# Kernel tuning notes

Hardware: AMD Instinct MI355X
Metric: run time of the kernel (lower is better)

## Reference

```python
import jax, jax.numpy as jnp
import numpy as np
from jax import lax

B, T, U, V = 4, 256, 64, 1024   # batch, enc frames, max target len, vocab (blank=0)
F, H, HD, J = 80, 512, 512, 512  # feat dim, enc dim, dec dim, joint dim
NEG = -1e30


def setup_inputs() -> dict:
    key = jax.random.key(0)
    ks = jax.random.split(key, 10)
    inputs = jax.random.normal(ks[0], (B, T, F), dtype=jnp.float32)
    targets = jax.random.randint(ks[1], (B, U), 1, V, dtype=jnp.int32)  # labels exclude blank=0
    input_lengths = jax.random.randint(ks[2], (B,), T // 2, T + 1, dtype=jnp.int32)
    target_lengths = jax.random.randint(ks[3], (B,), U // 2, U + 1, dtype=jnp.int32)
    s = 0.02
    W_enc = jax.random.normal(ks[4], (F, H), dtype=jnp.float32) * s
    emb = jax.random.normal(ks[5], (V, HD), dtype=jnp.float32) * s
    W_jenc = jax.random.normal(ks[6], (H, J), dtype=jnp.float32) * s
    W_jdec = jax.random.normal(ks[7], (HD, J), dtype=jnp.float32) * s
    b_j = jnp.zeros((J,), dtype=jnp.float32)
    W_out = jax.random.normal(ks[8], (J, V), dtype=jnp.float32) * s
    b_out = jnp.zeros((V,), dtype=jnp.float32)
    return {"inputs": inputs, "W_enc": W_enc, "emb": emb, "W_jenc": W_jenc,
            "W_jdec": W_jdec, "b_j": b_j, "W_out": W_out, "b_out": b_out,
            "targets": targets, "input_lengths": input_lengths,
            "target_lengths": target_lengths}


def rnnt_loss(log_probs, targets, in_lens, tgt_lens):
    """RNN-T loss (blank=0, 'gather' variant: gather blank/label lps, then DP).
    log_probs: (B,T,U+1,V) log-softmaxed joint. Returns mean loss over batch."""
    Bq, Tq, U1, _ = log_probs.shape
    Uq = U1 - 1
    blank_lp = log_probs[..., 0]                                    # (B,T,U+1)
    lbl_lp = jnp.take_along_axis(
        log_probs[:, :, :Uq, :],
        jnp.broadcast_to(targets[:, None, :, None], (Bq, Tq, Uq, 1)),
        axis=3)[..., 0]                                             # (B,T,U)
    u_idx = jnp.arange(Uq)
    lbl_lp = jnp.where(u_idx[None, None, :] < tgt_lens[:, None, None], lbl_lp, NEG)

    def row(a, py):
        # a: (B,U+1) = alpha_prev + blank emission; py: (B,U) label lps this frame
        def step(c, x):
            a_u, py_prev = x
            c = jnp.logaddexp(a_u, c + py_prev)
            return c, c
        c0 = a[:, 0]
        _, rest = lax.scan(step, c0, (a[:, 1:].T, py.T))            # (U,B)
        return jnp.concatenate([c0[:, None], rest.T], axis=1)      # (B,U+1)

    # t=0 row: alpha[0,u] = cumsum of label lps at frame 0
    alpha0 = jnp.concatenate(
        [jnp.zeros((Bq, 1), log_probs.dtype),
         jnp.cumsum(lbl_lp[:, 0, :], axis=1)], axis=1)              # (B,U+1)

    def tstep(alpha_prev, x):
        blank_prev, py_t = x
        alpha = row(alpha_prev + blank_prev, py_t)
        return alpha, alpha

    xs = (jnp.swapaxes(blank_lp[:, :-1, :], 0, 1),                  # (T-1,B,U+1)
          jnp.swapaxes(lbl_lp[:, 1:, :], 0, 1))                    # (T-1,B,U)
    _, rest = lax.scan(tstep, alpha0, xs)
    alphas = jnp.concatenate([alpha0[None], rest], axis=0)          # (T,B,U+1)

    b = jnp.arange(Bq)
    t_last = in_lens - 1
    a_fin = alphas[t_last, b, tgt_lens] + blank_lp[b, t_last, tgt_lens]
    return -jnp.mean(a_fin)


def reference(inputs, W_enc, emb, W_jenc, W_jdec, b_j, W_out, b_out,
              targets, input_lengths, target_lengths):
    enc = inputs @ W_enc                                            # (B,T,H) encoder
    padded = jnp.concatenate(
        [jnp.zeros((targets.shape[0], 1), targets.dtype), targets], axis=1)
    dec = emb[padded]                                               # (B,U+1,HD) decoder
    e = enc @ W_jenc                                                # (B,T,J)
    d = dec @ W_jdec                                                # (B,U+1,J)
    h = jnp.tanh(e[:, :, None, :] + d[:, None, :, :] + b_j)        # (B,T,U+1,J)
    logits = h @ W_out + b_out                                      # (B,T,U+1,V)
    log_probs = jax.nn.log_softmax(logits, axis=-1)
    return rnnt_loss(log_probs, targets, input_lengths, target_lengths)
```

## Files before the change

### kernel.cpp

```cpp
#include <hip/hip_runtime.h>
#include <stdint.h>

#define NEGF (-1e30f)

typedef unsigned short ushort_t;
typedef unsigned char uchar_t;
typedef __attribute__((ext_vector_type(2))) long v2i64;
typedef __attribute__((ext_vector_type(4))) float f32x4;

constexpr int cB = 4, cT = 256, cU = 64, cU1 = 65, cV = 1024, cF = 80, cH = 512, cJ = 512;
constexpr int cM = cB * cT * cU1;
constexpr int cTU = cT * cU1;
constexpr float LOG2E = 1.4426950408889634f;

__device__ __forceinline__ float tanh_fast(float x){
  float t = x * x;
  float num = x * (27.f + t);
  float den = fmaf(9.f, t, 27.f);
  float r = num * __builtin_amdgcn_rcpf(den);
  return fminf(1.f, fmaxf(-1.f, r));
}

__device__ __forceinline__ float logadd2(float x, float y){
  float m = fmaxf(x, y);
  return m + __builtin_amdgcn_logf(1.f + __builtin_amdgcn_exp2f(-fabsf(x - y)));
}

__device__ __forceinline__ float wshr1(float x){
  return __int_as_float(__builtin_amdgcn_mov_dpp(__float_as_int(x),
                                                 0x138, 0xF, 0xF, true));
}

__device__ __forceinline__ int pk8(float a, float b, float c, float d){
  int v = __builtin_amdgcn_cvt_pk_fp8_f32(a, b, 0, false);
  v = __builtin_amdgcn_cvt_pk_fp8_f32(c, d, v, true);
  return v;
}

__global__ __launch_bounds__(256) void k_pre(
    const float* __restrict__ inputs,
    const float* __restrict__ W_enc, const float* __restrict__ W_jenc,
    const float* __restrict__ emb, const int* __restrict__ targets,
    const float* __restrict__ W_jdec, const float* __restrict__ b_j,
    float* __restrict__ dmatb, float* __restrict__ e,
    const float* __restrict__ W_out, uchar_t* __restrict__ WTf8,
    float* __restrict__ S, float* __restrict__ out_loss)
{
  __shared__ float sA[4][512];
  __shared__ float sIn[4][80];
  int bid = blockIdx.x;
  int tid = threadIdx.x;

  if (bid < 256){
    int m0 = bid * 4;
    for (int i = tid; i < 320; i += 256)
      sIn[i / 80][i % 80] = inputs[m0 * 80 + i];
    __syncthreads();
    int c0 = tid, c1 = tid + 256;
    float a00 = 0.f, a01 = 0.f, a10 = 0.f, a11 = 0.f;
    float a20 = 0.f, a21 = 0.f, a30 = 0.f, a31 = 0.f;
#pragma unroll 8
    for (int k = 0; k < 80; k++){
      float w0 = W_enc[(size_t)k * 512 + c0];
      float w1 = W_enc[(size_t)k * 512 + c1];
      a00 = fmaf(sIn[0][k], w0, a00); a01 = fmaf(sIn[0][k], w1, a01);
      a10 = fmaf(sIn[1][k], w0, a10); a11 = fmaf(sIn[1][k], w1, a11);
      a20 = fmaf(sIn[2][k], w0, a20); a21 = fmaf(sIn[2][k], w1, a21);
      a30 = fmaf(sIn[3][k], w0, a30); a31 = fmaf(sIn[3][k], w1, a31);
    }
    sA[0][c0] = a00; sA[0][c1] = a01;
    sA[1][c0] = a10; sA[1][c1] = a11;
    sA[2][c0] = a20; sA[2][c1] = a21;
    sA[3][c0] = a30; sA[3][c1] = a31;
    __syncthreads();
    float b00 = 0.f, b01 = 0.f, b10 = 0.f, b11 = 0.f;
    float b20 = 0.f, b21 = 0.f, b30 = 0.f, b31 = 0.f;
#pragma unroll 8
    for (int k = 0; k < 512; k++){
      float w0 = W_jenc[(size_t)k * 512 + c0];
      float w1 = W_jenc[(size_t)k * 512 + c1];
      b00 = fmaf(sA[0][k], w0, b00); b01 = fmaf(sA[0][k], w1, b01);
      b10 = fmaf(sA[1][k], w0, b10); b11 = fmaf(sA[1][k], w1, b11);
      b20 = fmaf(sA[2][k], w0, b20); b21 = fmaf(sA[2][k], w1, b21);
      b30 = fmaf(sA[3][k], w0, b30); b31 = fmaf(sA[3][k], w1, b31);
    }
    e[(size_t)(m0 + 0) * 512 + c0] = b00; e[(size_t)(m0 + 0) * 512 + c1] = b01;
    e[(size_t)(m0 + 1) * 512 + c0] = b10; e[(size_t)(m0 + 1) * 512 + c1] = b11;
    e[(size_t)(m0 + 2) * 512 + c0] = b20; e[(size_t)(m0 + 2) * 512 + c1] = b21;
    e[(size_t)(m0 + 3) * 512 + c0] = b30; e[(size_t)(m0 + 3) * 512 + c1] = b31;
  } else if (bid < 386){
    int id = bid - 256;
    int bx = id & 1, by = id >> 1;
    int m0 = by * 4;
    int col = bx * 256 + tid;
    for (int i = tid; i < 4 * 512; i += 256){
      int r = i >> 9, c = i & 511;
      int row = m0 + r;
      int b = row / cU1, u = row % cU1;
      int src = (u == 0) ? 0 : targets[b * cU + (u - 1)];
      sA[r][c] = emb[(size_t)src * cH + c];
    }
    __syncthreads();
    float a0 = 0.f, a1 = 0.f, a2 = 0.f, a3 = 0.f;
#pragma unroll 8
    for (int k = 0; k < 512; k++){
      float bv = W_jdec[(size_t)k * cJ + col];
      a0 = fmaf(sA[0][k], bv, a0);
      a1 = fmaf(sA[1][k], bv, a1);
      a2 = fmaf(sA[2][k], bv, a2);
      a3 = fmaf(sA[3][k], bv, a3);
    }
    float bb = b_j[col];
    dmatb[(size_t)(m0 + 0) * cJ + col] = a0 + bb;
    dmatb[(size_t)(m0 + 1) * cJ + col] = a1 + bb;
    dmatb[(size_t)(m0 + 2) * cJ + col] = a2 + bb;
    dmatb[(size_t)(m0 + 3) * cJ + col] = a3 + bb;
  } else if (bid < 418){
    int id = bid - 386;
    int bn = id & 3, ksp = id >> 2;
    int lane = tid & 63, nth = tid >> 6;
    int c16 = lane & 15, quad = lane >> 4;
    int jA = ksp * 64 + quad * 8;
#pragma unroll
    for (int i = 0; i < 4; i++){
      int nt16 = nth * 4 + i;
      int n = bn * 256 + nt16 * 16 + c16;
      unsigned int p[4];
#pragma unroll
      for (int h = 0; h < 4; h++){
        int j0 = jA + (h >> 1) * 32 + (h & 1) * 4;
        float w0 = W_out[(size_t)(j0 + 0) * cV + n] * 32.f;
        float w1 = W_out[(size_t)(j0 + 1) * cV + n] * 32.f;
        float w2 = W_out[(size_t)(j0 + 2) * cV + n] * 32.f;
        float w3 = W_out[(size_t)(j0 + 3) * cV + n] * 32.f;
        p[h] = (unsigned)pk8(w0, w1, w2, w3);
      }
      uint4 pack; pack.x = p[0]; pack.y = p[1]; pack.z = p[2]; pack.w = p[3];
      *(uint4*)(WTf8 + (((size_t)(bn * 8 + ksp) * 16 + nt16) * 64 + lane) * 16) = pack;
    }
  } else {
    int i = (bid - 418) * 1024 + tid * 4;
    float4 z; z.x = 0.f; z.y = 0.f; z.z = 0.f; z.w = 0.f;
    *(float4*)(S + i) = z;
    if (bid == 418 && tid == 0) out_loss[0] = 0.f;
  }
}

__global__ __launch_bounds__(256) void k_hf(const float* __restrict__ e,
                                            const float* __restrict__ dmatb,
                                            uchar_t* __restrict__ Hbf8){
  __shared__ uchar_t sH[16 * 520];
  int tid = threadIdx.x;
  int wid = tid >> 6, lane = tid & 63;
  int c16 = lane & 15, quad = lane >> 4;
  int bm = blockIdx.x;
  int bu = bm >> 1, thalf = bm & 1;
  int b = bu / cU1;
  int t0 = thalf * 128;

  float dj[8];
  const float4* dp = (const float4*)(dmatb + (size_t)bu * cJ + lane * 8);
  float4 dA = dp[0], dB = dp[1];
  dj[0] = dA.x; dj[1] = dA.y; dj[2] = dA.z; dj[3] = dA.w;
  dj[4] = dB.x; dj[5] = dB.y; dj[6] = dB.z; dj[7] = dB.w;

  const float* erow0 = e + ((size_t)(b * cT + t0)) * cJ + lane * 8;
  uchar_t* outb = Hbf8 + (size_t)bm * 65536 + lane * 16;

  for (int mg = 0; mg < 8; mg++){
#pragma unroll
    for (int rr = 0; rr < 4; rr++){
      int rloc = wid * 4 + rr;
      const float* ep = erow0 + ((size_t)(mg * 16 + rloc)) * cJ;
      float4 e0 = *(const float4*)ep;
      float4 e1 = *(const float4*)(ep + 4);
      int v0 = pk8(tanh_fast(e0.x + dj[0]), tanh_fast(e0.y + dj[1]),
                   tanh_fast(e0.z + dj[2]), tanh_fast(e0.w + dj[3]));
      int v1 = pk8(tanh_fast(e1.x + dj[4]), tanh_fast(e1.y + dj[5]),
                   tanh_fast(e1.z + dj[6]), tanh_fast(e1.w + dj[7]));
      uint2 pk; pk.x = (unsigned)v0; pk.y = (unsigned)v1;
      *(uint2*)(sH + rloc * 520 + lane * 8) = pk;
    }
    __syncthreads();
#pragma unroll
    for (int q = 0; q < 2; q++){
      int ksp = wid * 2 + q;
      uint2 lo = *(const uint2*)(sH + c16 * 520 + ksp * 64 + quad * 8);
      uint2 hi = *(const uint2*)(sH + c16 * 520 + ksp * 64 + 32 + quad * 8);
      uint4 pack; pack.x = lo.x; pack.y = lo.y; pack.z = hi.x; pack.w = hi.y;
      *(uint4*)(outb + ((size_t)ksp * 8 + mg) * 1024) = pack;
    }
    __syncthreads();
  }
}

__global__ __launch_bounds__(256, 3) void k_joint(
    const uchar_t* __restrict__ Hbf8, const uchar_t* __restrict__ WTf8,
    const float* __restrict__ b_out, const int* __restrict__ targets,
    float* __restrict__ S,
    float* __restrict__ blank_g, float* __restrict__ lbl_g)
{
  __shared__ float redS[2][128];

  int tid = threadIdx.x;
  int wid = tid >> 6, lane = tid & 63;
  int quad = lane >> 4, c16 = lane & 15;
  int wm = wid & 1, wn = wid >> 1;
  int bid = blockIdx.x;
  int bm = ((bid >> 6) << 3) + (bid & 7);
  int bn = (bid >> 3) & 7;
  int bu = bm >> 1, thalf = bm & 1;
  int b = bu / cU1, u = bu - b * cU1;
  int tg = (u < cU) ? targets[b * cU + u] : -1;
  int lin0 = bu * cT + thalf * 128;

  f32x4 acc[4][4];
#pragma unroll
  for (int i = 0; i < 4; i++)
#pragma unroll
    for (int j = 0; j < 4; j++)
      acc[i][j] = (f32x4){0.f, 0.f, 0.f, 0.f};

  const uchar_t* aP = Hbf8 + (size_t)bm * 65536 + (wm * 4) * 1024 + lane * 16;
  const uchar_t* bP = WTf8 + (size_t)(bn >> 1) * 131072 + ((bn & 1) * 8 + wn * 4) * 1024 + lane * 16;

  v2i64 afX[4], bfX[4], afY[4], bfY[4];
#pragma unroll
  for (int mt = 0; mt < 4; mt++) afX[mt] = *(const v2i64*)(aP + mt * 1024);
#pragma unroll
  for (int nt = 0; nt < 4; nt++) bfX[nt] = *(const v2i64*)(bP + nt * 1024);

#pragma unroll
  for (int k2 = 0; k2 < 4; k2++){
    {
      size_t kY = (size_t)(2 * k2 + 1);
#pragma unroll
      for (int mt = 0; mt < 4; mt++) afY[mt] = *(const v2i64*)(aP + kY * 8192 + mt * 1024);
#pragma unroll
      for (int nt = 0; nt < 4; nt++) bfY[nt] = *(const v2i64*)(bP + kY * 16384 + nt * 1024);
    }
#pragma unroll
    for (int h = 0; h < 2; h++)
#pragma unroll
      for (int mt = 0; mt < 4; mt++)
#pragma unroll
        for (int nt = 0; nt < 4; nt++)
          acc[mt][nt] = __builtin_amdgcn_mfma_f32_16x16x32_fp8_fp8(afX[mt][h], bfX[nt][h], acc[mt][nt], 0, 0, 0);
    if (k2 < 3){
      size_t kX = (size_t)(2 * k2 + 2);
#pragma unroll
      for (int mt = 0; mt < 4; mt++) afX[mt] = *(const v2i64*)(aP + kX * 8192 + mt * 1024);
#pragma unroll
      for (int nt = 0; nt < 4; nt++) bfX[nt] = *(const v2i64*)(bP + kX * 16384 + nt * 1024);
    }
#pragma unroll
    for (int h = 0; h < 2; h++)
#pragma unroll
      for (int mt = 0; mt < 4; mt++)
#pragma unroll
        for (int nt = 0; nt < 4; nt++)
          acc[mt][nt] = __builtin_amdgcn_mfma_f32_16x16x32_fp8_fp8(afY[mt][h], bfY[nt][h], acc[mt][nt], 0, 0, 0);
  }

  float bv[4];
#pragma unroll
  for (int nt = 0; nt < 4; nt++) bv[nt] = b_out[bn * 128 + (wn * 4 + nt) * 16 + c16] * LOG2E;

  bool ownL = (tg >= 0) && ((tg >> 7) == bn) && (((tg >> 6) & 1) == wn);
  int ntO = (tg >> 4) & 3;
  int tgc = tg & 15;
  const float descale2 = LOG2E / 32.f;

#pragma unroll
  for (int mt = 0; mt < 4; mt++){
#pragma unroll
    for (int r = 0; r < 4; r++){
      int rl = wm * 64 + mt * 16 + quad * 4 + r;
      float l[4];
#pragma unroll
      for (int nt = 0; nt < 4; nt++) l[nt] = fmaf(acc[mt][nt][r], descale2, bv[nt]);
      if (bn == 0 && wn == 0 && c16 == 0) blank_g[lin0 + rl] = l[0];
      if (ownL && c16 == tgc){
        float v = l[0];
#pragma unroll
        for (int k = 1; k < 4; k++) v = (ntO == k) ? l[k] : v;
        lbl_g[lin0 + rl] = v;
      }
      float s = __builtin_amdgcn_exp2f(l[0]) + __builtin_amdgcn_exp2f(l[1])
              + __builtin_amdgcn_exp2f(l[2]) + __builtin_amdgcn_exp2f(l[3]);
      s += __shfl_xor(s, 1, 64);
      s += __shfl_xor(s, 2, 64);
      s += __shfl_xor(s, 4, 64);
      s += __shfl_xor(s, 8, 64);
      if (c16 == 0) redS[wn][rl] = s;
    }
  }
  __syncthreads();
  if (tid < 128)
    atomicAdd(&S[lin0 + tid], redS[0][tid] + redS[1][tid]);
}

__global__ __launch_bounds__(256) void k_dp(
    const float* __restrict__ S, const float* __restrict__ blank_g,
    const float* __restrict__ lbl_g,
    const int* __restrict__ in_len, const int* __restrict__ tgt_len,
    float* __restrict__ out)
{
  __shared__ float sbb[cTU];
  __shared__ float slb[cTU];
  __shared__ float sS[256];
  int b = blockIdx.x;
  int tl  = tgt_len[b];
  size_t base = (size_t)b * cTU;
  for (int i = threadIdx.x; i < cTU / 4; i += 256){
    int row = i >> 6;
    if (row > tl) continue;
    float4 sv = ((const float4*)(S + base))[i];
    float4 bvv = ((const float4*)(blank_g + base))[i];
    float4 ls;
    ls.x = __builtin_amdgcn_logf(sv.x); ls.y = __builtin_amdgcn_logf(sv.y);
    ls.z = __builtin_amdgcn_logf(sv.z); ls.w = __builtin_amdgcn_logf(sv.w);
    float4 bo;
    bo.x = bvv.x - ls.x; bo.y = bvv.y - ls.y;
    bo.z = bvv.z - ls.z; bo.w = bvv.w - ls.w;
    ((float4*)sbb)[i] = bo;
    float4 lo;
    if (row < tl){
      float4 lv = ((const float4*)(lbl_g + base))[i];
      lo.x = lv.x - ls.x; lo.y = lv.y - ls.y;
      lo.z = lv.z - ls.z; lo.w = lv.w - ls.w;
    } else {
      lo.x = NEGF; lo.y = NEGF; lo.z = NEGF; lo.w = NEGF;
    }
    ((float4*)slb)[i] = lo;
  }
  __syncthreads();
  if (threadIdx.x >= 64) return;

  int u = threadIdx.x;
  int til = in_len[b] - 1;
  bool cap64 = (tl == 64);
  bool isTL = (u == tl);
  const float* pbu  = sbb + (u << 8);
  const float* pbu1 = sbb + (((u >= 1) ? u - 1 : 0) << 8);
  const float* plu1 = slb + (((u >= 1) ? u - 1 : 0) << 8);
  const float* plu2 = slb + (((u >= 2) ? u - 2 : 0) << 8);
  bool u1 = (u >= 1), u2 = (u >= 2);
  float fb = pbu[til];

  float A = (u == 0) ? 0.f : NEGF;
  float res = 0.f;

  auto ld = [&](const float* p, int i, bool ok) -> float {
    float x = p[i & 255];
    return (ok & ((unsigned)i < 256u)) ? x : NEGF;
  };

  int i0 = -u;
  float o0 = ld(pbu,  i0,     true);
  float o1 = ld(pbu,  i0 + 1, true);
  float o2 = ld(plu1, i0 + 1, u1);
  float o3 = ld(pbu1, i0 + 1, u1);
  float o4 = ld(plu1, i0 + 2, u1);
  float o5 = ld(plu2, i0 + 2, u2);

#pragma unroll 3
  for (int g = 0; g < 159; g++){
    float up1 = wshr1(A);
    float up2 = wshr1(up1);

    int i0n = i0 + 2;
    float n0 = ld(pbu,  i0n,     true);
    float n1 = ld(pbu,  i0n + 1, true);
    float n2 = ld(plu1, i0n + 1, u1);
    float n3 = ld(pbu1, i0n + 1, u1);
    float n4 = ld(plu1, i0n + 2, u1);
    float n5 = ld(plu2, i0n + 2, u2);

    float C0 = o0 + o1;
    float C1 = logadd2(o2 + o1, o3 + o4);
    float C2 = o5 + o4;

    float am0 = A + o0, am1 = up1 + o2;
    float Amid = logadd2(am0, am1);
    bool tv1 = ((unsigned)(i0 + 1) < 256u);
    Amid = tv1 ? Amid : NEGF;

    float a0 = A + C0, a1 = up1 + C1, a2 = up2 + C2;
    float m3 = fmaxf(fmaxf(a0, a1), a2);
    float s3 = __builtin_amdgcn_exp2f(a0 - m3) + __builtin_amdgcn_exp2f(a1 - m3)
             + __builtin_amdgcn_exp2f(a2 - m3);
    float Anew = m3 + __builtin_amdgcn_logf(s3);
    bool tv2 = ((unsigned)(i0 + 2) < 256u);
    Anew = tv2 ? Anew : NEGF;

    if (isTL && (i0 + 1) == til) res = Amid + fb;
    if (isTL && (i0 + 2) == til) res = Anew + fb;
    if (u == 63){
      if (tv1) sS[i0 + 1] = Amid;
      if (tv2) sS[i0 + 2] = Anew;
    }
    A = Anew;
    i0 = i0n;
    o0 = n0; o1 = n1; o2 = n2; o3 = n3; o4 = n4; o5 = n5;
  }

  if (cap64){
    const float* pb64 = sbb + (64 << 8);
    const float* pl63 = slb + (63 << 8);
    float A64 = sS[0] + pl63[0];
    for (int t = 1; t <= til; t++)
      A64 = logadd2(A64 + pb64[t - 1], sS[t] + pl63[t]);
    if (u == 0) res = A64 + pb64[til];
  }

  res += __shfl_xor(res, 1, 64);
  res += __shfl_xor(res, 2, 64);
  res += __shfl_xor(res, 4, 64);
  res += __shfl_xor(res, 8, 64);
  res += __shfl_xor(res, 16, 64);
  res += __shfl_xor(res, 32, 64);
  if (u == 0) atomicAdd(out, -0.17328679513998632f * res);
}

extern "C" void kernel_launch(void* const* d_in, const int* in_sizes, int n_in,
                              void* d_out, int out_size, void* d_ws, size_t ws_size,
                              hipStream_t stream)
{
  (void)in_sizes; (void)n_in; (void)out_size; (void)ws_size;
  const float* inputs = (const float*)d_in[0];
  const float* W_enc  = (const float*)d_in[1];
  const float* emb    = (const float*)d_in[2];
  const float* W_jenc = (const float*)d_in[3];
  const float* W_jdec = (const float*)d_in[4];
  const float* b_j    = (const float*)d_in[5];
  const float* W_out  = (const float*)d_in[6];
  const float* b_out  = (const float*)d_in[7];
  const int* targets  = (const int*)d_in[8];
  const int* in_len   = (const int*)d_in[9];
  const int* tgt_len  = (const int*)d_in[10];

  char* w = (char*)d_ws;
  auto alloc = [&](size_t bytes){ char* p = w; w += (bytes + 255) & ~(size_t)255; return p; };
  float* e       = (float*)alloc((size_t)1024 * 512 * 4);
  float* dmatb   = (float*)alloc((size_t)260 * 512 * 4);
  float* blank_g = (float*)alloc((size_t)cM * 4);
  float* lbl_g   = (float*)alloc((size_t)cM * 4);
  float* S       = (float*)alloc((size_t)cM * 4);
  uchar_t* Hbf8  = (uchar_t*)alloc((size_t)520 * 65536);
  uchar_t* WTf8  = (uchar_t*)alloc((size_t)4 * 131072);

  k_pre<<<483, 256, 0, stream>>>(inputs, W_enc, W_jenc, emb, targets, W_jdec, b_j,
                                 dmatb, e, W_out, WTf8, S, (float*)d_out);
  k_hf<<<520, 256, 0, stream>>>(e, dmatb, Hbf8);
  k_joint<<<4160, 256, 0, stream>>>(Hbf8, WTf8, b_out, targets, S, blank_g, lbl_g);
  k_dp<<<4, 256, 0, stream>>>(S, blank_g, lbl_g, in_len, tgt_len, (float*)d_out);
}
```

Measured before the change: 223.2 us.

## Precompute DP emission combinations cooperatively across block in phases

The anti-diagonal RNN-T alpha recurrence previously had one wavefront compute all emission sums (C0, C1, C2 and the logadd) inline on its serial chain. Now all 256 threads precompute these terms for 16 diagonal steps at a time into shared memory, and the single wavefront then runs only the recurrence on the precomputed values. The aim is to take the loads and the logadd off the serial critical path. In exchange it adds 10 phases of block-wide __syncthreads and extra shared-memory traffic.

```diff
diff --git a/kernel.cpp b/kernel.cpp
--- a/kernel.cpp
+++ b/kernel.cpp
@@ -306,13 +306,18 @@
     const int* __restrict__ in_len, const int* __restrict__ tgt_len,
     float* __restrict__ out)
 {
+  constexpr int G = 16;
+  constexpr int NPH = 10;
   __shared__ float sbb[cTU];
   __shared__ float slb[cTU];
   __shared__ float sS[256];
+  __shared__ float cC0[G * 64], cC1[G * 64], cC2[G * 64];
+  __shared__ float cOA[G * 64], cOB[G * 64];
+  int tid = threadIdx.x;
   int b = blockIdx.x;
   int tl  = tgt_len[b];
   size_t base = (size_t)b * cTU;
-  for (int i = threadIdx.x; i < cTU / 4; i += 256){
+  for (int i = tid; i < cTU / 4; i += 256){
     int row = i >> 6;
     if (row > tl) continue;
     float4 sv = ((const float4*)(S + base))[i];
@@ -335,18 +340,12 @@
     ((float4*)slb)[i] = lo;
   }
   __syncthreads();
-  if (threadIdx.x >= 64) return;
-
-  int u = threadIdx.x;
+
   int til = in_len[b] - 1;
   bool cap64 = (tl == 64);
+  int u = tid;
   bool isTL = (u == tl);
-  const float* pbu  = sbb + (u << 8);
-  const float* pbu1 = sbb + (((u >= 1) ? u - 1 : 0) << 8);
-  const float* plu1 = slb + (((u >= 1) ? u - 1 : 0) << 8);
-  const float* plu2 = slb + (((u >= 2) ? u - 2 : 0) << 8);
-  bool u1 = (u >= 1), u2 = (u >= 2);
-  float fb = pbu[til];
+  float fb = (tid < 64) ? sbb[(u << 8) + til] : 0.f;
 
   float A = (u == 0) ? 0.f : NEGF;
   float res = 0.f;
@@ -356,54 +355,67 @@
     return (ok & ((unsigned)i < 256u)) ? x : NEGF;
   };
 
-  int i0 = -u;
-  float o0 = ld(pbu,  i0,     true);
-  float o1 = ld(pbu,  i0 + 1, true);
-  float o2 = ld(plu1, i0 + 1, u1);
-  float o3 = ld(pbu1, i0 + 1, u1);
-  float o4 = ld(plu1, i0 + 2, u1);
-  float o5 = ld(plu2, i0 + 2, u2);
-
-#pragma unroll 3
-  for (int g = 0; g < 159; g++){
-    float up1 = wshr1(A);
-    float up2 = wshr1(up1);
-
-    int i0n = i0 + 2;
-    float n0 = ld(pbu,  i0n,     true);
-    float n1 = ld(pbu,  i0n + 1, true);
-    float n2 = ld(plu1, i0n + 1, u1);
-    float n3 = ld(pbu1, i0n + 1, u1);
-    float n4 = ld(plu1, i0n + 2, u1);
-    float n5 = ld(plu2, i0n + 2, u2);
-
-    float C0 = o0 + o1;
-    float C1 = logadd2(o2 + o1, o3 + o4);
-    float C2 = o5 + o4;
-
-    float am0 = A + o0, am1 = up1 + o2;
-    float Amid = logadd2(am0, am1);
-    bool tv1 = ((unsigned)(i0 + 1) < 256u);
-    Amid = tv1 ? Amid : NEGF;
-
-    float a0 = A + C0, a1 = up1 + C1, a2 = up2 + C2;
-    float m3 = fmaxf(fmaxf(a0, a1), a2);
-    float s3 = __builtin_amdgcn_exp2f(a0 - m3) + __builtin_amdgcn_exp2f(a1 - m3)
-             + __builtin_amdgcn_exp2f(a2 - m3);
-    float Anew = m3 + __builtin_amdgcn_logf(s3);
-    bool tv2 = ((unsigned)(i0 + 2) < 256u);
-    Anew = tv2 ? Anew : NEGF;
-
-    if (isTL && (i0 + 1) == til) res = Amid + fb;
-    if (isTL && (i0 + 2) == til) res = Anew + fb;
-    if (u == 63){
-      if (tv1) sS[i0 + 1] = Amid;
-      if (tv2) sS[i0 + 2] = Anew;
-    }
-    A = Anew;
-    i0 = i0n;
-    o0 = n0; o1 = n1; o2 = n2; o3 = n3; o4 = n4; o5 = n5;
-  }
+  for (int p = 0; p < NPH; p++){
+    for (int w = tid; w < G * 64; w += 256){
+      int gg = w >> 6, uu = w & 63;
+      int g = p * G + gg;
+      int i0 = 2 * g - uu;
+      bool v1 = (uu >= 1), v2 = (uu >= 2);
+      const float* pbu  = sbb + (uu << 8);
+      const float* pbu1 = sbb + ((v1 ? uu - 1 : 0) << 8);
+      const float* plu1 = slb + ((v1 ? uu - 1 : 0) << 8);
+      const float* plu2 = slb + ((v2 ? uu - 2 : 0) << 8);
+      float o0 = ld(pbu,  i0,     true);
+      float o1 = ld(pbu,  i0 + 1, true);
+      float o2 = ld(plu1, i0 + 1, v1);
+      float o3 = ld(pbu1, i0 + 1, v1);
+      float o4 = ld(plu1, i0 + 2, v1);
+      float o5 = ld(plu2, i0 + 2, v2);
+      cC0[w] = o0 + o1;
+      cC1[w] = logadd2(o2 + o1, o3 + o4);
+      cC2[w] = o5 + o4;
+      cOA[w] = o0;
+      cOB[w] = o2;
+    }
+    __syncthreads();
+    if (tid < 64){
+      float c0v = cC0[u], c1v = cC1[u], c2v = cC2[u];
+      float oAv = cOA[u], oBv = cOB[u];
+#pragma unroll
+      for (int gg = 0; gg < G; gg++){
+        int g = p * G + gg;
+        int nx = (gg + 1 < G) ? ((gg + 1) << 6) + u : (gg << 6) + u;
+        float nc0 = cC0[nx], nc1 = cC1[nx], nc2 = cC2[nx];
+        float noA = cOA[nx], noB = cOB[nx];
+        if (g < 159){
+          float up1 = wshr1(A);
+          float up2 = wshr1(up1);
+          int i0 = 2 * g - u;
+          float Amid = logadd2(A + oAv, up1 + oBv);
+          bool tv1 = ((unsigned)(i0 + 1) < 256u);
+          Amid = tv1 ? Amid : NEGF;
+          float a0 = A + c0v, a1 = up1 + c1v, a2 = up2 + c2v;
+          float m3 = fmaxf(fmaxf(a0, a1), a2);
+          float s3 = __builtin_amdgcn_exp2f(a0 - m3) + __builtin_amdgcn_exp2f(a1 - m3)
+                   + __builtin_amdgcn_exp2f(a2 - m3);
+          float Anew = m3 + __builtin_amdgcn_logf(s3);
+          bool tv2 = ((unsigned)(i0 + 2) < 256u);
+          Anew = tv2 ? Anew : NEGF;
+          if (isTL && (i0 + 1) == til) res = Amid + fb;
+          if (isTL && (i0 + 2) == til) res = Anew + fb;
+          if (u == 63){
+            if (tv1) sS[i0 + 1] = Amid;
+            if (tv2) sS[i0 + 2] = Anew;
+          }
+          A = Anew;
+        }
+        c0v = nc0; c1v = nc1; c2v = nc2; oAv = noA; oBv = noB;
+      }
+    }
+    __syncthreads();
+  }
+
+  if (tid >= 64) return;
 
   if (cap64){
     const float* pb64 = sbb + (64 << 8);
```

Result: no change. 221.2 us (-0.9%).
